# Kernel optimization log

Measured on AMD Instinct MI355X. Metric: run time of the kernel, lower is better.

## Reference

```python
import jax, jax.numpy as jnp
import numpy as np

U, I, K = 100000, 50000, 64
N_II_LAYERS = 2
N_UI_LAYERS = 3
EPS = 1e-12  # torch F.normalize default eps


def spmm(src, dst, w, x, n):
    # out[dst] += w * x[src]  (COO sparse-dense matmul, LGConv with normalize=False)
    return jax.ops.segment_sum(x[src] * w[:, None], dst, num_segments=n)


def l2norm(x):
    # torch.nn.functional.normalize(x, p=2, dim=1)
    return x / jnp.maximum(jnp.linalg.norm(x, axis=1, keepdims=True), EPS)


def setup_inputs() -> dict:
    key = jax.random.key(0)
    ks = jax.random.split(key, 9)
    E_II, E_UI = 1600000, 4800000
    return {
        "Gu": jax.random.normal(ks[0], (U, K), dtype=jnp.float32),
        "Gi": jax.random.normal(ks[1], (I, K), dtype=jnp.float32),
        "Gis": jax.random.normal(ks[2], (I, K), dtype=jnp.float32),
        "ii_w": jax.random.uniform(ks[3], (E_II,), dtype=jnp.float32),
        "ui_w": jax.random.uniform(ks[4], (E_UI,), dtype=jnp.float32),
        "ii_src": jax.random.randint(ks[5], (E_II,), 0, I, dtype=jnp.int32),
        "ii_dst": jax.random.randint(ks[6], (E_II,), 0, I, dtype=jnp.int32),
        "ui_src": jax.random.randint(ks[7], (E_UI,), 0, U + I, dtype=jnp.int32),
        "ui_dst": jax.random.randint(ks[8], (E_UI,), 0, U + I, dtype=jnp.int32),
    }


def reference(Gu, Gi, Gis, ii_w, ui_w, ii_src, ii_dst, ui_src, ui_dst):
    # item-item propagation (n_ii_layers LGConv, no per-layer norm)
    gis = Gis
    for _ in range(N_II_LAYERS):
        gis = spmm(ii_src, ii_dst, ii_w, gis, I)
    # user-item propagation with per-layer L2 normalize
    ego = jnp.concatenate([Gu, Gi], axis=0)  # [U+I, K]
    all_emb = [ego]
    for layer in range(N_UI_LAYERS):
        all_emb.append(l2norm(spmm(ui_src, ui_dst, ui_w, all_emb[layer], U + I)))
    mean_emb = jnp.mean(jnp.stack(all_emb, axis=1), axis=1)  # [U+I, K]
    gu, gi = mean_emb[:U], mean_emb[U:]
    return gu, gi + l2norm(gis)
```

## Files before the change

kernel.cpp:

```cpp
#include <hip/hip_runtime.h>
#include <hip/hip_bf16.h>

constexpr int U_N = 100000;
constexpr int I_N = 50000;
constexpr int KDIM = 64;
constexpr float EPSF = 1e-12f;

constexpr int RPB = 256;
constexpr int BSHIFT = 8;
constexpr int CH = 4096;

typedef float f4 __attribute__((ext_vector_type(4)));
typedef unsigned short u16;

__device__ inline f4 ld4(const float* p) { return *(const f4*)p; }

__device__ inline unsigned pack_bf16(float a, float b) {
    unsigned ua = __float_as_uint(a);
    unsigned ub = __float_as_uint(b);
    ua += 0x7fffu + ((ua >> 16) & 1u);
    ub += 0x7fffu + ((ub >> 16) & 1u);
    return (ua >> 16) | (ub & 0xffff0000u);
}

__device__ inline void bf8_to_f32(uint4 u, float* f) {
    unsigned w0 = u.x, w1 = u.y, w2 = u.z, w3 = u.w;
    f[0] = __uint_as_float(w0 << 16);  f[1] = __uint_as_float(w0 & 0xffff0000u);
    f[2] = __uint_as_float(w1 << 16);  f[3] = __uint_as_float(w1 & 0xffff0000u);
    f[4] = __uint_as_float(w2 << 16);  f[5] = __uint_as_float(w2 & 0xffff0000u);
    f[6] = __uint_as_float(w3 << 16);  f[7] = __uint_as_float(w3 & 0xffff0000u);
}

__global__ void bhist_k(const int* __restrict__ dst, int* __restrict__ cnt, int E, int NB) {
    __shared__ int h[1024];
    int t = threadIdx.x;
    for (int i = t; i < 1024; i += 256) h[i] = 0;
    __syncthreads();
    int stride = gridDim.x * 256 * 4;
    for (int i = (blockIdx.x * 256 + t) * 4; i < E; i += stride) {
        if (i + 4 <= E) {
            int4 d = *(const int4*)(dst + i);
            atomicAdd(&h[d.x >> BSHIFT], 1);
            atomicAdd(&h[d.y >> BSHIFT], 1);
            atomicAdd(&h[d.z >> BSHIFT], 1);
            atomicAdd(&h[d.w >> BSHIFT], 1);
        } else {
            for (int k = i; k < E; ++k) atomicAdd(&h[dst[k] >> BSHIFT], 1);
        }
    }
    __syncthreads();
    for (int i = t; i < NB; i += 256) if (h[i]) atomicAdd(&cnt[i], h[i]);
}

__global__ void bscan_k(const int* __restrict__ cnt, int* __restrict__ base,
                        int* __restrict__ cur, int NB) {
    __shared__ int s[1024];
    int t = threadIdx.x;
    int c = (t < NB) ? cnt[t] : 0;
    s[t] = c;
    __syncthreads();
    for (int off = 1; off < 1024; off <<= 1) {
        int v = s[t] + ((t >= off) ? s[t - off] : 0);
        __syncthreads();
        s[t] = v;
        __syncthreads();
    }
    int ex = s[t] - c;
    if (t < NB) { base[t] = ex; cur[t] = ex; }
    if (t == NB - 1) base[NB] = s[t];
}

__global__ __launch_bounds__(1024) void bpart_k(
        const int* __restrict__ src, const int* __restrict__ dst,
        const float* __restrict__ w, int* __restrict__ gcur,
        int2* __restrict__ pairs, unsigned char* __restrict__ dlo,
        int E, int NB) {
    __shared__ int hist[1024];
    __shared__ int sA[1024];
    __shared__ int rb[1024];
    __shared__ int2 stp[CH];
    __shared__ unsigned stg[CH];
    int t = threadIdx.x;
    int nch = (E + CH - 1) / CH;
    for (int c = blockIdx.x; c < nch; c += gridDim.x) {
        int cb = c * CH;
        int n = min(CH, E - cb);
        hist[t] = 0;
        __syncthreads();
        int esrc[4], ew[4], ebkt[4], edlo[4];
        bool ev[4];
#pragma unroll
        for (int k = 0; k < 4; ++k) {
            int j = k * 1024 + t;
            ev[k] = j < n;
            if (ev[k]) {
                int i = cb + j;
                int d = dst[i];
                esrc[k] = src[i];
                ew[k] = __float_as_int(w[i]);
                ebkt[k] = d >> BSHIFT;
                edlo[k] = d & (RPB - 1);
                atomicAdd(&hist[ebkt[k]], 1);
            }
        }
        __syncthreads();
        int cnt_t = hist[t];
        sA[t] = cnt_t;
        __syncthreads();
        for (int off = 1; off < 1024; off <<= 1) {
            int v = sA[t] + ((t >= off) ? sA[t - off] : 0);
            __syncthreads();
            sA[t] = v;
            __syncthreads();
        }
        sA[t] -= cnt_t;
        if (t < NB && cnt_t > 0) rb[t] = atomicAdd(&gcur[t], cnt_t);
        hist[t] = 0;
        __syncthreads();
#pragma unroll
        for (int k = 0; k < 4; ++k) {
            if (ev[k]) {
                int b = ebkt[k];
                int local = atomicAdd(&hist[b], 1);
                int pos = sA[b] + local;
                stp[pos] = make_int2(esrc[k], ew[k]);
                stg[pos] = (unsigned)(rb[b] + local) | ((unsigned)edlo[k] << 24);
            }
        }
        __syncthreads();
#pragma unroll
        for (int k = 0; k < 4; ++k) {
            int p = k * 1024 + t;
            if (p < n) {
                unsigned g = stg[p];
                unsigned ga = g & 0xFFFFFFu;
                pairs[ga] = stp[p];
                dlo[ga] = (unsigned char)(g >> 24);
            }
        }
        __syncthreads();
    }
}

__global__ __launch_bounds__(1024) void bfill_k(
        const int* __restrict__ base, const int2* __restrict__ pairs,
        const unsigned char* __restrict__ dlo, int2* __restrict__ e2,
        int* __restrict__ start, int NB, int Nrows) {
    __shared__ int hist[RPB];
    __shared__ int pos[RPB + 1];
    int t = threadIdx.x;
    for (int b = blockIdx.x; b < NB; b += gridDim.x) {
        int gb = base[b];
        int cnt = base[b + 1] - gb;
        if (t < RPB) hist[t] = 0;
        __syncthreads();
        for (int i = t; i < cnt; i += 1024) atomicAdd(&hist[dlo[gb + i]], 1);
        __syncthreads();
        if (t < RPB) pos[t] = hist[t];
        __syncthreads();
        for (int off = 1; off < RPB; off <<= 1) {
            int v = 0;
            if (t < RPB) v = pos[t] + ((t >= off) ? pos[t - off] : 0);
            __syncthreads();
            if (t < RPB) pos[t] = v;
            __syncthreads();
        }
        int myv = 0;
        if (t < RPB) myv = (t == 0) ? 0 : pos[t - 1];
        __syncthreads();
        if (t < RPB) pos[t] = myv;
        if (t == 0) pos[RPB] = cnt;
        __syncthreads();
        int r0 = b * RPB;
        if (t <= RPB) {
            int row = r0 + t;
            if (row <= Nrows) start[row] = gb + pos[t];
        }
        __syncthreads();
        for (int i = t; i < cnt; i += 1024) {
            int r = dlo[gb + i];
            int p = atomicAdd(&pos[r], 1);
            e2[gb + p] = pairs[gb + i];
        }
        __syncthreads();
    }
}


__device__ inline float group8_sum(float v) {
    v += __shfl_xor(v, 1, 64);
    v += __shfl_xor(v, 2, 64);
    v += __shfl_xor(v, 4, 64);
    return v;
}

__device__ inline void spmm_row_bf(const int2* __restrict__ e2, int j0, int j1,
                                   const u16* __restrict__ x, int g, int l,
                                   float a[8]) {
    float a0[8] = {0, 0, 0, 0, 0, 0, 0, 0};
    float a1[8] = {0, 0, 0, 0, 0, 0, 0, 0};
    int j = j0;
    for (; j + 16 <= j1; j += 16) {
        int2 ea = e2[j + g];
        int2 eb = e2[j + 8 + g];
        uint4 ua = *(const uint4*)(x + (size_t)ea.x * KDIM + l * 8);
        uint4 ub = *(const uint4*)(x + (size_t)eb.x * KDIM + l * 8);
        float wa = __int_as_float(ea.y), wb = __int_as_float(eb.y);
        float fa[8], fb[8];
        bf8_to_f32(ua, fa);
        bf8_to_f32(ub, fb);
#pragma unroll
        for (int c = 0; c < 8; ++c) {
            a0[c] += wa * fa[c];
            a1[c] += wb * fb[c];
        }
    }
    for (; j < j1; j += 8) {
        if (j + g < j1) {
            int2 ea = e2[j + g];
            uint4 ua = *(const uint4*)(x + (size_t)ea.x * KDIM + l * 8);
            float wa = __int_as_float(ea.y);
            float fa[8];
            bf8_to_f32(ua, fa);
#pragma unroll
            for (int c = 0; c < 8; ++c) a0[c] += wa * fa[c];
        }
    }
#pragma unroll
    for (int c = 0; c < 8; ++c) {
        float v = a0[c] + a1[c];
        v += __shfl_xor(v, 8, 64);
        v += __shfl_xor(v, 16, 64);
        v += __shfl_xor(v, 32, 64);
        a[c] = v;
    }
}

__global__ void cvt_bf8(const float* __restrict__ in, u16* __restrict__ out, int n8) {
    int i = blockIdx.x * blockDim.x + threadIdx.x;
    if (i >= n8) return;
    f4 v0 = ld4(in + (size_t)i * 8);
    f4 v1 = ld4(in + (size_t)i * 8 + 4);
    uint4 pk;
    pk.x = pack_bf16(v0.x, v0.y);
    pk.y = pack_bf16(v0.z, v0.w);
    pk.z = pack_bf16(v1.x, v1.y);
    pk.w = pack_bf16(v1.z, v1.w);
    *(uint4*)(out + (size_t)i * 8) = pk;
}

__global__ void spmm_pull_bf(const int* __restrict__ start, const int2* __restrict__ e2,
                             const u16* __restrict__ x, u16* __restrict__ y, int nrows) {
    const int lane = threadIdx.x & 63;
    const int g = lane >> 3, l = lane & 7;
    const int r = (blockIdx.x * blockDim.x + threadIdx.x) >> 6;
    if (r >= nrows) return;
    float a[8];
    spmm_row_bf(e2, start[r], start[r + 1], x, g, l, a);
    if (g == 0) {
        uint4 pk;
        pk.x = pack_bf16(a[0], a[1]);
        pk.y = pack_bf16(a[2], a[3]);
        pk.z = pack_bf16(a[4], a[5]);
        pk.w = pack_bf16(a[6], a[7]);
        *(uint4*)(y + (size_t)r * KDIM + l * 8) = pk;
    }
}

__global__ void spmm_pull_f32(const int* __restrict__ start, const int2* __restrict__ e2,
                              const u16* __restrict__ x, float* __restrict__ y, int nrows) {
    const int lane = threadIdx.x & 63;
    const int g = lane >> 3, l = lane & 7;
    const int r = (blockIdx.x * blockDim.x + threadIdx.x) >> 6;
    if (r >= nrows) return;
    float a[8];
    spmm_row_bf(e2, start[r], start[r + 1], x, g, l, a);
    if (g == 0) {
        float* yp = y + (size_t)r * KDIM + l * 8;
        *(f4*)yp = f4{a[0], a[1], a[2], a[3]};
        *(f4*)(yp + 4) = f4{a[4], a[5], a[6], a[7]};
    }
}

__global__ void spmm_pull_norm_noacc(const int* __restrict__ start, const int2* __restrict__ e2,
                                     const u16* __restrict__ x, u16* __restrict__ cur,
                                     int nrows) {
    const int lane = threadIdx.x & 63;
    const int g = lane >> 3, l = lane & 7;
    const int r = (blockIdx.x * blockDim.x + threadIdx.x) >> 6;
    if (r >= nrows) return;
    float a[8];
    spmm_row_bf(e2, start[r], start[r + 1], x, g, l, a);
    float loc = 0.f;
#pragma unroll
    for (int c = 0; c < 8; ++c) loc += a[c] * a[c];
    float ss = group8_sum(loc);
    float inv = 1.f / fmaxf(sqrtf(ss), EPSF);
    if (g == 0) {
        uint4 pk;
        pk.x = pack_bf16(a[0] * inv, a[1] * inv);
        pk.y = pack_bf16(a[2] * inv, a[3] * inv);
        pk.z = pack_bf16(a[4] * inv, a[5] * inv);
        pk.w = pack_bf16(a[6] * inv, a[7] * inv);
        *(uint4*)(cur + (size_t)r * KDIM + l * 8) = pk;
    }
}

__global__ void spmm_pull_norm_final(const int* __restrict__ start, const int2* __restrict__ e2,
                                     const u16* __restrict__ x,
                                     const u16* __restrict__ n1,
                                     const float* __restrict__ Gu,
                                     const float* __restrict__ Gi,
                                     const float* __restrict__ gis,
                                     float* __restrict__ out, int nrows) {
    const int lane = threadIdx.x & 63;
    const int g = lane >> 3, l = lane & 7;
    const int r = (blockIdx.x * blockDim.x + threadIdx.x) >> 6;
    if (r >= nrows) return;
    float a[8];
    spmm_row_bf(e2, start[r], start[r + 1], x, g, l, a);
    float loc = 0.f;
#pragma unroll
    for (int c = 0; c < 8; ++c) loc += a[c] * a[c];
    float ss = group8_sum(loc);
    float inv = 1.f / fmaxf(sqrtf(ss), EPSF);
    if (g != 0) return;
    const float* ep = (r < U_N) ? Gu + (size_t)r * KDIM + l * 8
                                : Gi + (size_t)(r - U_N) * KDIM + l * 8;
    f4 e0 = __builtin_nontemporal_load((const f4*)ep);
    f4 e1 = __builtin_nontemporal_load((const f4*)(ep + 4));
    uint4 u1 = *(const uint4*)(n1 + (size_t)r * KDIM + l * 8);
    uint4 u2 = *(const uint4*)(x + (size_t)r * KDIM + l * 8);
    float f1[8], f2[8];
    bf8_to_f32(u1, f1);
    bf8_to_f32(u2, f2);
    f4 v0 = (e0 + f4{f1[0], f1[1], f1[2], f1[3]} + f4{f2[0], f2[1], f2[2], f2[3]}
                + f4{a[0] * inv, a[1] * inv, a[2] * inv, a[3] * inv}) * 0.25f;
    f4 v1 = (e1 + f4{f1[4], f1[5], f1[6], f1[7]} + f4{f2[4], f2[5], f2[6], f2[7]}
                + f4{a[4] * inv, a[5] * inv, a[6] * inv, a[7] * inv}) * 0.25f;
    if (r >= U_N) {
        const float* gp = gis + (size_t)(r - U_N) * KDIM + l * 8;
        f4 g0 = ld4(gp);
        f4 g1 = ld4(gp + 4);
        float loc2 = g0.x * g0.x + g0.y * g0.y + g0.z * g0.z + g0.w * g0.w
                   + g1.x * g1.x + g1.y * g1.y + g1.z * g1.z + g1.w * g1.w;
        float ss2 = group8_sum(loc2);
        float inv2 = 1.f / fmaxf(sqrtf(ss2), EPSF);
        v0 += g0 * inv2;
        v1 += g1 * inv2;
    }
    float* op = out + (size_t)r * KDIM + l * 8;
    __builtin_nontemporal_store(v0, (f4*)op);
    __builtin_nontemporal_store(v1, (f4*)(op + 4));
}

extern "C" void kernel_launch(void* const* d_in, const int* in_sizes, int n_in,
                              void* d_out, int out_size, void* d_ws, size_t ws_size,
                              hipStream_t stream) {
    const float* Gu     = (const float*)d_in[0];
    const float* Gi     = (const float*)d_in[1];
    const float* Gis    = (const float*)d_in[2];
    const float* ii_w   = (const float*)d_in[3];
    const float* ui_w   = (const float*)d_in[4];
    const int*   ii_src = (const int*)d_in[5];
    const int*   ii_dst = (const int*)d_in[6];
    const int*   ui_src = (const int*)d_in[7];
    const int*   ui_dst = (const int*)d_in[8];
    const int E_II = in_sizes[5];
    const int E_UI = in_sizes[7];

    const int NR    = U_N + I_N;
    const size_t NI = (size_t)I_N * KDIM;
    const size_t NA = (size_t)NR * KDIM;

    u16*  bufA = (u16*)d_ws;
    u16*  bufB = bufA + NA;
    u16*  gis0 = bufB + NA;
    u16*  gisA = gis0 + NI;
    float* gisB = (float*)(gisA + NI);
    int2*  ui_e = (int2*)(gisB + NI);
    int2*  ii_e = ui_e + E_UI;
    int*   ui_start = (int*)(ii_e + E_II);
    int*   ii_start = ui_start + (NR + 1);
    int*   bkt_cnt  = ii_start + (I_N + 1);
    int*   bkt_base = bkt_cnt + 1024;
    int*   bkt_cur  = bkt_base + 1056;

    int2*          pairs_s = (int2*)bufA;
    unsigned char* dlo_s   = (unsigned char*)gis0;

    float* out = (float*)d_out;

    const int NB_UI = (NR + RPB - 1) / RPB;
    const int NB_II = (I_N + RPB - 1) / RPB;

    hipMemsetAsync(bkt_cnt, 0, NB_UI * sizeof(int), stream);
    bhist_k<<<1024, 256, 0, stream>>>(ui_dst, bkt_cnt, E_UI, NB_UI);
    bscan_k<<<1, 1024, 0, stream>>>(bkt_cnt, bkt_base, bkt_cur, NB_UI);
    bpart_k<<<512, 1024, 0, stream>>>(ui_src, ui_dst, ui_w, bkt_cur, pairs_s, dlo_s, E_UI, NB_UI);
    bfill_k<<<256, 1024, 0, stream>>>(bkt_base, pairs_s, dlo_s, ui_e, ui_start, NB_UI, NR);

    hipMemsetAsync(bkt_cnt, 0, NB_II * sizeof(int), stream);
    bhist_k<<<1024, 256, 0, stream>>>(ii_dst, bkt_cnt, E_II, NB_II);
    bscan_k<<<1, 1024, 0, stream>>>(bkt_cnt, bkt_base, bkt_cur, NB_II);
    bpart_k<<<512, 1024, 0, stream>>>(ii_src, ii_dst, ii_w, bkt_cur, pairs_s, dlo_s, E_II, NB_II);
    bfill_k<<<256, 1024, 0, stream>>>(bkt_base, pairs_s, dlo_s, ii_e, ii_start, NB_II, I_N);

    cvt_bf8<<<(int)((NI / 8 + 255) / 256), 256, 0, stream>>>(Gis, gis0, (int)(NI / 8));
    spmm_pull_bf<<<(I_N + 3) / 4, 256, 0, stream>>>(ii_start, ii_e, gis0, gisA, I_N);
    spmm_pull_f32<<<(I_N + 3) / 4, 256, 0, stream>>>(ii_start, ii_e, gisA, gisB, I_N);

    const int nu8 = (int)((size_t)U_N * KDIM / 8);
    const int ni8 = (int)(NI / 8);
    cvt_bf8<<<(nu8 + 255) / 256, 256, 0, stream>>>(Gu, bufA, nu8);
    cvt_bf8<<<(ni8 + 255) / 256, 256, 0, stream>>>(Gi, bufA + (size_t)U_N * KDIM, ni8);

    spmm_pull_norm_noacc<<<(NR + 3) / 4, 256, 0, stream>>>(ui_start, ui_e, bufA, bufB, NR);
    spmm_pull_norm_noacc<<<(NR + 3) / 4, 256, 0, stream>>>(ui_start, ui_e, bufB, bufA, NR);
    spmm_pull_norm_final<<<(NR + 3) / 4, 256, 0, stream>>>(ui_start, ui_e, bufA, bufB,
                                                           Gu, Gi, gisB, out, NR);
}
```

Measured before the change: 686.6 us.

## Fuse item-item and user-item SpMM layers into shared launches; unroll gather deeper

```diff
diff --git a/kernel.cpp b/kernel.cpp
--- a/kernel.cpp
+++ b/kernel.cpp
@@ -11,9 +11,21 @@
 constexpr int CH = 4096;
 
 typedef float f4 __attribute__((ext_vector_type(4)));
+typedef int   i2v __attribute__((ext_vector_type(2)));
+typedef unsigned uv4 __attribute__((ext_vector_type(4)));
 typedef unsigned short u16;
 
 __device__ inline f4 ld4(const float* p) { return *(const f4*)p; }
+
+__device__ inline i2v ntl_e(const int2* p) {
+    return __builtin_nontemporal_load((const i2v*)p);
+}
+__device__ inline uv4 ntl_u4(const u16* p) {
+    return __builtin_nontemporal_load((const uv4*)p);
+}
+__device__ inline f4 ntl_f4(const float* p) {
+    return __builtin_nontemporal_load((const f4*)p);
+}
 
 __device__ inline unsigned pack_bf16(float a, float b) {
     unsigned ua = __float_as_uint(a);
@@ -23,12 +35,18 @@
     return (ua >> 16) | (ub & 0xffff0000u);
 }
 
-__device__ inline void bf8_to_f32(uint4 u, float* f) {
-    unsigned w0 = u.x, w1 = u.y, w2 = u.z, w3 = u.w;
-    f[0] = __uint_as_float(w0 << 16);  f[1] = __uint_as_float(w0 & 0xffff0000u);
-    f[2] = __uint_as_float(w1 << 16);  f[3] = __uint_as_float(w1 & 0xffff0000u);
-    f[4] = __uint_as_float(w2 << 16);  f[5] = __uint_as_float(w2 & 0xffff0000u);
-    f[6] = __uint_as_float(w3 << 16);  f[7] = __uint_as_float(w3 & 0xffff0000u);
+__device__ inline void bf8_to_f32(uv4 u, float* f) {
+    f[0] = __uint_as_float(u[0] << 16);  f[1] = __uint_as_float(u[0] & 0xffff0000u);
+    f[2] = __uint_as_float(u[1] << 16);  f[3] = __uint_as_float(u[1] & 0xffff0000u);
+    f[4] = __uint_as_float(u[2] << 16);  f[5] = __uint_as_float(u[2] & 0xffff0000u);
+    f[6] = __uint_as_float(u[3] << 16);  f[7] = __uint_as_float(u[3] & 0xffff0000u);
+}
+
+__device__ inline void fma8(float A[8], float w, uv4 u) {
+    float f[8];
+    bf8_to_f32(u, f);
+#pragma unroll
+    for (int c = 0; c < 8; ++c) A[c] += w * f[c];
 }
 
 __global__ void bhist_k(const int* __restrict__ dst, int* __restrict__ cnt, int E, int NB) {
@@ -194,41 +212,47 @@
     return v;
 }
 
-__device__ inline void spmm_row_bf(const int2* __restrict__ e2, int j0, int j1,
+__device__ inline void spmm_row_bf(const int2* __restrict__ e2p, int j0, int j1,
                                    const u16* __restrict__ x, int g, int l,
                                    float a[8]) {
-    float a0[8] = {0, 0, 0, 0, 0, 0, 0, 0};
-    float a1[8] = {0, 0, 0, 0, 0, 0, 0, 0};
+    float A0[8] = {0, 0, 0, 0, 0, 0, 0, 0};
+    float A1[8] = {0, 0, 0, 0, 0, 0, 0, 0};
+    float A2[8] = {0, 0, 0, 0, 0, 0, 0, 0};
+    float A3[8] = {0, 0, 0, 0, 0, 0, 0, 0};
     int j = j0;
-    for (; j + 16 <= j1; j += 16) {
-        int2 ea = e2[j + g];
-        int2 eb = e2[j + 8 + g];
-        uint4 ua = *(const uint4*)(x + (size_t)ea.x * KDIM + l * 8);
-        uint4 ub = *(const uint4*)(x + (size_t)eb.x * KDIM + l * 8);
-        float wa = __int_as_float(ea.y), wb = __int_as_float(eb.y);
-        float fa[8], fb[8];
-        bf8_to_f32(ua, fa);
-        bf8_to_f32(ub, fb);
-#pragma unroll
-        for (int c = 0; c < 8; ++c) {
-            a0[c] += wa * fa[c];
-            a1[c] += wb * fb[c];
-        }
+    for (; j + 32 <= j1; j += 32) {
+        i2v e0 = ntl_e(e2p + j + g);
+        i2v e1 = ntl_e(e2p + j + 8 + g);
+        i2v e2 = ntl_e(e2p + j + 16 + g);
+        i2v e3 = ntl_e(e2p + j + 24 + g);
+        uv4 u0 = *(const uv4*)(x + (size_t)e0.x * KDIM + l * 8);
+        uv4 u1 = *(const uv4*)(x + (size_t)e1.x * KDIM + l * 8);
+        uv4 u2 = *(const uv4*)(x + (size_t)e2.x * KDIM + l * 8);
+        uv4 u3 = *(const uv4*)(x + (size_t)e3.x * KDIM + l * 8);
+        fma8(A0, __int_as_float(e0.y), u0);
+        fma8(A1, __int_as_float(e1.y), u1);
+        fma8(A2, __int_as_float(e2.y), u2);
+        fma8(A3, __int_as_float(e3.y), u3);
+    }
+    if (j + 16 <= j1) {
+        i2v e0 = ntl_e(e2p + j + g);
+        i2v e1 = ntl_e(e2p + j + 8 + g);
+        uv4 u0 = *(const uv4*)(x + (size_t)e0.x * KDIM + l * 8);
+        uv4 u1 = *(const uv4*)(x + (size_t)e1.x * KDIM + l * 8);
+        fma8(A0, __int_as_float(e0.y), u0);
+        fma8(A1, __int_as_float(e1.y), u1);
+        j += 16;
     }
     for (; j < j1; j += 8) {
         if (j + g < j1) {
-            int2 ea = e2[j + g];
-            uint4 ua = *(const uint4*)(x + (size_t)ea.x * KDIM + l * 8);
-            float wa = __int_as_float(ea.y);
-            float fa[8];
-            bf8_to_f32(ua, fa);
-#pragma unroll
-            for (int c = 0; c < 8; ++c) a0[c] += wa * fa[c];
+            i2v e0 = ntl_e(e2p + j + g);
+            uv4 u0 = *(const uv4*)(x + (size_t)e0.x * KDIM + l * 8);
+            fma8(A2, __int_as_float(e0.y), u0);
         }
     }
 #pragma unroll
     for (int c = 0; c < 8; ++c) {
-        float v = a0[c] + a1[c];
+        float v = (A0[c] + A1[c]) + (A2[c] + A3[c]);
         v += __shfl_xor(v, 8, 64);
         v += __shfl_xor(v, 16, 64);
         v += __shfl_xor(v, 32, 64);
@@ -236,73 +260,98 @@
     }
 }
 
-__global__ void cvt_bf8(const float* __restrict__ in, u16* __restrict__ out, int n8) {
+__global__ void cvt_all(const float* __restrict__ Gu, const float* __restrict__ Gi,
+                        const float* __restrict__ Gis, u16* __restrict__ bufA,
+                        u16* __restrict__ gis0, int nu8, int na8, int ntot8) {
     int i = blockIdx.x * blockDim.x + threadIdx.x;
-    if (i >= n8) return;
-    f4 v0 = ld4(in + (size_t)i * 8);
-    f4 v1 = ld4(in + (size_t)i * 8 + 4);
-    uint4 pk;
-    pk.x = pack_bf16(v0.x, v0.y);
-    pk.y = pack_bf16(v0.z, v0.w);
-    pk.z = pack_bf16(v1.x, v1.y);
-    pk.w = pack_bf16(v1.z, v1.w);
-    *(uint4*)(out + (size_t)i * 8) = pk;
-}
-
-__global__ void spmm_pull_bf(const int* __restrict__ start, const int2* __restrict__ e2,
-                             const u16* __restrict__ x, u16* __restrict__ y, int nrows) {
+    if (i >= ntot8) return;
+    const float* p;
+    u16* o;
+    if (i < nu8)      { p = Gu  + (size_t)i * 8;          o = bufA + (size_t)i * 8; }
+    else if (i < na8) { p = Gi  + (size_t)(i - nu8) * 8;  o = bufA + (size_t)i * 8; }
+    else              { p = Gis + (size_t)(i - na8) * 8;  o = gis0 + (size_t)(i - na8) * 8; }
+    f4 v0 = ld4(p);
+    f4 v1 = ld4(p + 4);
+    uv4 pk;
+    pk[0] = pack_bf16(v0.x, v0.y);
+    pk[1] = pack_bf16(v0.z, v0.w);
+    pk[2] = pack_bf16(v1.x, v1.y);
+    pk[3] = pack_bf16(v1.z, v1.w);
+    *(uv4*)o = pk;
+}
+
+__global__ void spmm_fused_l1(const int* __restrict__ ui_start, const int2* __restrict__ ui_e,
+                              const u16* __restrict__ xu, u16* __restrict__ yu,
+                              const int* __restrict__ ii_start, const int2* __restrict__ ii_e,
+                              const u16* __restrict__ xi, u16* __restrict__ yi,
+                              int nui, int nii) {
     const int lane = threadIdx.x & 63;
     const int g = lane >> 3, l = lane & 7;
     const int r = (blockIdx.x * blockDim.x + threadIdx.x) >> 6;
-    if (r >= nrows) return;
-    float a[8];
-    spmm_row_bf(e2, start[r], start[r + 1], x, g, l, a);
-    if (g == 0) {
-        uint4 pk;
-        pk.x = pack_bf16(a[0], a[1]);
-        pk.y = pack_bf16(a[2], a[3]);
-        pk.z = pack_bf16(a[4], a[5]);
-        pk.w = pack_bf16(a[6], a[7]);
-        *(uint4*)(y + (size_t)r * KDIM + l * 8) = pk;
-    }
-}
-
-__global__ void spmm_pull_f32(const int* __restrict__ start, const int2* __restrict__ e2,
-                              const u16* __restrict__ x, float* __restrict__ y, int nrows) {
+    if (r < nui) {
+        float a[8];
+        spmm_row_bf(ui_e, ui_start[r], ui_start[r + 1], xu, g, l, a);
+        float loc = 0.f;
+#pragma unroll
+        for (int c = 0; c < 8; ++c) loc += a[c] * a[c];
+        float ss = group8_sum(loc);
+        float inv = 1.f / fmaxf(sqrtf(ss), EPSF);
+        if (g == 0) {
+            uv4 pk;
+            pk[0] = pack_bf16(a[0] * inv, a[1] * inv);
+            pk[1] = pack_bf16(a[2] * inv, a[3] * inv);
+            pk[2] = pack_bf16(a[4] * inv, a[5] * inv);
+            pk[3] = pack_bf16(a[6] * inv, a[7] * inv);
+            *(uv4*)(yu + (size_t)r * KDIM + l * 8) = pk;
+        }
+    } else if (r < nui + nii) {
+        int rr = r - nui;
+        float a[8];
+        spmm_row_bf(ii_e, ii_start[rr], ii_start[rr + 1], xi, g, l, a);
+        if (g == 0) {
+            uv4 pk;
+            pk[0] = pack_bf16(a[0], a[1]);
+            pk[1] = pack_bf16(a[2], a[3]);
+            pk[2] = pack_bf16(a[4], a[5]);
+            pk[3] = pack_bf16(a[6], a[7]);
+            *(uv4*)(yi + (size_t)rr * KDIM + l * 8) = pk;
+        }
+    }
+}
+
+__global__ void spmm_fused_l2(const int* __restrict__ ui_start, const int2* __restrict__ ui_e,
+                              const u16* __restrict__ xu, u16* __restrict__ yu,
+                              const int* __restrict__ ii_start, const int2* __restrict__ ii_e,
+                              const u16* __restrict__ xi, float* __restrict__ yi,
+                              int nui, int nii) {
     const int lane = threadIdx.x & 63;
     const int g = lane >> 3, l = lane & 7;
     const int r = (blockIdx.x * blockDim.x + threadIdx.x) >> 6;
-    if (r >= nrows) return;
-    float a[8];
-    spmm_row_bf(e2, start[r], start[r + 1], x, g, l, a);
-    if (g == 0) {
-        float* yp = y + (size_t)r * KDIM + l * 8;
-        *(f4*)yp = f4{a[0], a[1], a[2], a[3]};
-        *(f4*)(yp + 4) = f4{a[4], a[5], a[6], a[7]};
-    }
-}
-
-__global__ void spmm_pull_norm_noacc(const int* __restrict__ start, const int2* __restrict__ e2,
-                                     const u16* __restrict__ x, u16* __restrict__ cur,
-                                     int nrows) {
-    const int lane = threadIdx.x & 63;
-    const int g = lane >> 3, l = lane & 7;
-    const int r = (blockIdx.x * blockDim.x + threadIdx.x) >> 6;
-    if (r >= nrows) return;
-    float a[8];
-    spmm_row_bf(e2, start[r], start[r + 1], x, g, l, a);
-    float loc = 0.f;
-#pragma unroll
-    for (int c = 0; c < 8; ++c) loc += a[c] * a[c];
-    float ss = group8_sum(loc);
-    float inv = 1.f / fmaxf(sqrtf(ss), EPSF);
-    if (g == 0) {
-        uint4 pk;
-        pk.x = pack_bf16(a[0] * inv, a[1] * inv);
-        pk.y = pack_bf16(a[2] * inv, a[3] * inv);
-        pk.z = pack_bf16(a[4] * inv, a[5] * inv);
-        pk.w = pack_bf16(a[6] * inv, a[7] * inv);
-        *(uint4*)(cur + (size_t)r * KDIM + l * 8) = pk;
+    if (r < nui) {
+        float a[8];
+        spmm_row_bf(ui_e, ui_start[r], ui_start[r + 1], xu, g, l, a);
+        float loc = 0.f;
+#pragma unroll
+        for (int c = 0; c < 8; ++c) loc += a[c] * a[c];
+        float ss = group8_sum(loc);
+        float inv = 1.f / fmaxf(sqrtf(ss), EPSF);
+        if (g == 0) {
+            uv4 pk;
+            pk[0] = pack_bf16(a[0] * inv, a[1] * inv);
+            pk[1] = pack_bf16(a[2] * inv, a[3] * inv);
+            pk[2] = pack_bf16(a[4] * inv, a[5] * inv);
+            pk[3] = pack_bf16(a[6] * inv, a[7] * inv);
+            *(uv4*)(yu + (size_t)r * KDIM + l * 8) = pk;
+        }
+    } else if (r < nui + nii) {
+        int rr = r - nui;
+        float a[8];
+        spmm_row_bf(ii_e, ii_start[rr], ii_start[rr + 1], xi, g, l, a);
+        if (g == 0) {
+            float* yp = yi + (size_t)rr * KDIM + l * 8;
+            *(f4*)yp = f4{a[0], a[1], a[2], a[3]};
+            *(f4*)(yp + 4) = f4{a[4], a[5], a[6], a[7]};
+        }
     }
 }
 
@@ -327,10 +376,10 @@
     if (g != 0) return;
     const float* ep = (r < U_N) ? Gu + (size_t)r * KDIM + l * 8
                                 : Gi + (size_t)(r - U_N) * KDIM + l * 8;
-    f4 e0 = __builtin_nontemporal_load((const f4*)ep);
-    f4 e1 = __builtin_nontemporal_load((const f4*)(ep + 4));
-    uint4 u1 = *(const uint4*)(n1 + (size_t)r * KDIM + l * 8);
-    uint4 u2 = *(const uint4*)(x + (size_t)r * KDIM + l * 8);
+    f4 e0 = ntl_f4(ep);
+    f4 e1 = ntl_f4(ep + 4);
+    uv4 u1 = ntl_u4(n1 + (size_t)r * KDIM + l * 8);
+    uv4 u2 = *(const uv4*)(x + (size_t)r * KDIM + l * 8);
     float f1[8], f2[8];
     bf8_to_f32(u1, f1);
     bf8_to_f32(u2, f2);
@@ -340,8 +389,8 @@
                 + f4{a[4] * inv, a[5] * inv, a[6] * inv, a[7] * inv}) * 0.25f;
     if (r >= U_N) {
         const float* gp = gis + (size_t)(r - U_N) * KDIM + l * 8;
-        f4 g0 = ld4(gp);
-        f4 g1 = ld4(gp + 4);
+        f4 g0 = ntl_f4(gp);
+        f4 g1 = ntl_f4(gp + 4);
         float loc2 = g0.x * g0.x + g0.y * g0.y + g0.z * g0.z + g0.w * g0.w
                    + g1.x * g1.x + g1.y * g1.y + g1.z * g1.z + g1.w * g1.w;
         float ss2 = group8_sum(loc2);
@@ -406,17 +455,16 @@
     bpart_k<<<512, 1024, 0, stream>>>(ii_src, ii_dst, ii_w, bkt_cur, pairs_s, dlo_s, E_II, NB_II);
     bfill_k<<<256, 1024, 0, stream>>>(bkt_base, pairs_s, dlo_s, ii_e, ii_start, NB_II, I_N);
 
-    cvt_bf8<<<(int)((NI / 8 + 255) / 256), 256, 0, stream>>>(Gis, gis0, (int)(NI / 8));
-    spmm_pull_bf<<<(I_N + 3) / 4, 256, 0, stream>>>(ii_start, ii_e, gis0, gisA, I_N);
-    spmm_pull_f32<<<(I_N + 3) / 4, 256, 0, stream>>>(ii_start, ii_e, gisA, gisB, I_N);
-
     const int nu8 = (int)((size_t)U_N * KDIM / 8);
-    const int ni8 = (int)(NI / 8);
-    cvt_bf8<<<(nu8 + 255) / 256, 256, 0, stream>>>(Gu, bufA, nu8);
-    cvt_bf8<<<(ni8 + 255) / 256, 256, 0, stream>>>(Gi, bufA + (size_t)U_N * KDIM, ni8);
-
-    spmm_pull_norm_noacc<<<(NR + 3) / 4, 256, 0, stream>>>(ui_start, ui_e, bufA, bufB, NR);
-    spmm_pull_norm_noacc<<<(NR + 3) / 4, 256, 0, stream>>>(ui_start, ui_e, bufB, bufA, NR);
+    const int na8 = (int)(NA / 8);
+    const int nt8 = (int)((NA + NI) / 8);
+    cvt_all<<<(nt8 + 255) / 256, 256, 0, stream>>>(Gu, Gi, Gis, bufA, gis0, nu8, na8, nt8);
+
+    const int NTOT = NR + I_N;
+    spmm_fused_l1<<<(NTOT + 3) / 4, 256, 0, stream>>>(ui_start, ui_e, bufA, bufB,
+                                                      ii_start, ii_e, gis0, gisA, NR, I_N);
+    spmm_fused_l2<<<(NTOT + 3) / 4, 256, 0, stream>>>(ui_start, ui_e, bufB, bufA,
+                                                      ii_start, ii_e, gisA, gisB, NR, I_N);
     spmm_pull_norm_final<<<(NR + 3) / 4, 256, 0, stream>>>(ui_start, ui_e, bufA, bufB,
                                                            Gu, Gi, gisB, out, NR);
 }
```

Measured after the change: 829.1 us. 20.8% more time.

## Batch UI and II CSR construction into shared launches and pack row index into weight bits

Applied to the files above, without the earlier changes.

```diff
diff --git a/kernel.cpp b/kernel.cpp
--- a/kernel.cpp
+++ b/kernel.cpp
@@ -31,13 +31,18 @@
     f[6] = __uint_as_float(w3 << 16);  f[7] = __uint_as_float(w3 & 0xffff0000u);
 }
 
-__global__ void bhist_k(const int* __restrict__ dst, int* __restrict__ cnt, int E, int NB) {
+__global__ void bhist2_k(const int* __restrict__ dstU, int* __restrict__ cntU, int EU, int NBu,
+                         const int* __restrict__ dstI, int* __restrict__ cntI, int EI, int NBi,
+                         int GU, int GTOT) {
+    const int* dst; int* cnt; int E; int NB; int nbk; int bid;
+    if ((int)blockIdx.x < GU) { dst = dstU; cnt = cntU; E = EU; NB = NBu; nbk = GU; bid = blockIdx.x; }
+    else { dst = dstI; cnt = cntI; E = EI; NB = NBi; nbk = GTOT - GU; bid = blockIdx.x - GU; }
     __shared__ int h[1024];
     int t = threadIdx.x;
     for (int i = t; i < 1024; i += 256) h[i] = 0;
     __syncthreads();
-    int stride = gridDim.x * 256 * 4;
-    for (int i = (blockIdx.x * 256 + t) * 4; i < E; i += stride) {
+    int stride = nbk * 256 * 4;
+    for (int i = (bid * 256 + t) * 4; i < E; i += stride) {
         if (i + 4 <= E) {
             int4 d = *(const int4*)(dst + i);
             atomicAdd(&h[d.x >> BSHIFT], 1);
@@ -52,11 +57,13 @@
     for (int i = t; i < NB; i += 256) if (h[i]) atomicAdd(&cnt[i], h[i]);
 }
 
-__global__ void bscan_k(const int* __restrict__ cnt, int* __restrict__ base,
-                        int* __restrict__ cur, int NB) {
+__global__ void bscan2_k(const int* __restrict__ cntU, int* __restrict__ baseU,
+                         int* __restrict__ curU, int NBu,
+                         const int* __restrict__ cntI, int* __restrict__ baseI,
+                         int* __restrict__ curI, int NBi) {
     __shared__ int s[1024];
     int t = threadIdx.x;
-    int c = (t < NB) ? cnt[t] : 0;
+    int c = (t < NBu) ? cntU[t] : 0;
     s[t] = c;
     __syncthreads();
     for (int off = 1; off < 1024; off <<= 1) {
@@ -65,29 +72,47 @@
         s[t] = v;
         __syncthreads();
     }
-    int ex = s[t] - c;
-    if (t < NB) { base[t] = ex; cur[t] = ex; }
-    if (t == NB - 1) base[NB] = s[t];
-}
-
-__global__ __launch_bounds__(1024) void bpart_k(
-        const int* __restrict__ src, const int* __restrict__ dst,
-        const float* __restrict__ w, int* __restrict__ gcur,
-        int2* __restrict__ pairs, unsigned char* __restrict__ dlo,
-        int E, int NB) {
+    if (t < NBu) { baseU[t] = s[t] - c; curU[t] = s[t] - c; }
+    if (t == NBu - 1) baseU[NBu] = s[t];
+    __syncthreads();
+    int c2 = (t < NBi) ? cntI[t] : 0;
+    s[t] = c2;
+    __syncthreads();
+    for (int off = 1; off < 1024; off <<= 1) {
+        int v = s[t] + ((t >= off) ? s[t - off] : 0);
+        __syncthreads();
+        s[t] = v;
+        __syncthreads();
+    }
+    if (t < NBi) { baseI[t] = s[t] - c2; curI[t] = s[t] - c2; }
+    if (t == NBi - 1) baseI[NBi] = s[t];
+}
+
+__global__ __launch_bounds__(1024) void bpart2_k(
+        const int* __restrict__ srcU, const int* __restrict__ dstU,
+        const float* __restrict__ wU, int* __restrict__ curU,
+        int2* __restrict__ pairsU, int nchU, int EU,
+        const int* __restrict__ srcI, const int* __restrict__ dstI,
+        const float* __restrict__ wI, int* __restrict__ curI,
+        int2* __restrict__ pairsI, int nchI, int EI) {
     __shared__ int hist[1024];
     __shared__ int sA[1024];
     __shared__ int rb[1024];
     __shared__ int2 stp[CH];
     __shared__ unsigned stg[CH];
     int t = threadIdx.x;
-    int nch = (E + CH - 1) / CH;
-    for (int c = blockIdx.x; c < nch; c += gridDim.x) {
-        int cb = c * CH;
+    int ntot = nchU + nchI;
+    for (int c = blockIdx.x; c < ntot; c += gridDim.x) {
+        const int* src; const int* dst; const float* w; int* gcur; int2* pairs;
+        int cb, E;
+        if (c < nchU) { src = srcU; dst = dstU; w = wU; gcur = curU; pairs = pairsU;
+                        cb = c * CH; E = EU; }
+        else          { src = srcI; dst = dstI; w = wI; gcur = curI; pairs = pairsI;
+                        cb = (c - nchU) * CH; E = EI; }
         int n = min(CH, E - cb);
         hist[t] = 0;
         __syncthreads();
-        int esrc[4], ew[4], ebkt[4], edlo[4];
+        int esrc[4], ew[4], ebkt[4];
         bool ev[4];
 #pragma unroll
         for (int k = 0; k < 4; ++k) {
@@ -97,9 +122,8 @@
                 int i = cb + j;
                 int d = dst[i];
                 esrc[k] = src[i];
-                ew[k] = __float_as_int(w[i]);
+                ew[k] = (int)((__float_as_uint(w[i]) & 0xFFFFFF00u) | (unsigned)(d & (RPB - 1)));
                 ebkt[k] = d >> BSHIFT;
-                edlo[k] = d & (RPB - 1);
                 atomicAdd(&hist[ebkt[k]], 1);
             }
         }
@@ -114,7 +138,7 @@
             __syncthreads();
         }
         sA[t] -= cnt_t;
-        if (t < NB && cnt_t > 0) rb[t] = atomicAdd(&gcur[t], cnt_t);
+        if (cnt_t > 0) rb[t] = atomicAdd(&gcur[t], cnt_t);
         hist[t] = 0;
         __syncthreads();
 #pragma unroll
@@ -124,37 +148,39 @@
                 int local = atomicAdd(&hist[b], 1);
                 int pos = sA[b] + local;
                 stp[pos] = make_int2(esrc[k], ew[k]);
-                stg[pos] = (unsigned)(rb[b] + local) | ((unsigned)edlo[k] << 24);
+                stg[pos] = (unsigned)(rb[b] + local);
             }
         }
         __syncthreads();
 #pragma unroll
         for (int k = 0; k < 4; ++k) {
             int p = k * 1024 + t;
-            if (p < n) {
-                unsigned g = stg[p];
-                unsigned ga = g & 0xFFFFFFu;
-                pairs[ga] = stp[p];
-                dlo[ga] = (unsigned char)(g >> 24);
-            }
-        }
-        __syncthreads();
-    }
-}
-
-__global__ __launch_bounds__(1024) void bfill_k(
-        const int* __restrict__ base, const int2* __restrict__ pairs,
-        const unsigned char* __restrict__ dlo, int2* __restrict__ e2,
-        int* __restrict__ start, int NB, int Nrows) {
+            if (p < n) pairs[stg[p]] = stp[p];
+        }
+        __syncthreads();
+    }
+}
+
+__global__ __launch_bounds__(1024) void bfill2_k(
+        const int* __restrict__ baseU, const int2* __restrict__ pairsU,
+        int2* __restrict__ e2U, int* __restrict__ startU, int NBu, int NRu,
+        const int* __restrict__ baseI, const int2* __restrict__ pairsI,
+        int2* __restrict__ e2I, int* __restrict__ startI, int NBi, int NRi) {
     __shared__ int hist[RPB];
     __shared__ int pos[RPB + 1];
     int t = threadIdx.x;
-    for (int b = blockIdx.x; b < NB; b += gridDim.x) {
-        int gb = base[b];
-        int cnt = base[b + 1] - gb;
+    int ntot = NBu + NBi;
+    for (int b = blockIdx.x; b < ntot; b += gridDim.x) {
+        const int* base; const int2* pairs; int2* e2; int* start; int bb, Nrows;
+        if (b < NBu) { base = baseU; pairs = pairsU; e2 = e2U; start = startU;
+                       bb = b; Nrows = NRu; }
+        else         { base = baseI; pairs = pairsI; e2 = e2I; start = startI;
+                       bb = b - NBu; Nrows = NRi; }
+        int gb = base[bb];
+        int cnt = base[bb + 1] - gb;
         if (t < RPB) hist[t] = 0;
         __syncthreads();
-        for (int i = t; i < cnt; i += 1024) atomicAdd(&hist[dlo[gb + i]], 1);
+        for (int i = t; i < cnt; i += 1024) atomicAdd(&hist[pairs[gb + i].y & (RPB - 1)], 1);
         __syncthreads();
         if (t < RPB) pos[t] = hist[t];
         __syncthreads();
@@ -171,16 +197,17 @@
         if (t < RPB) pos[t] = myv;
         if (t == 0) pos[RPB] = cnt;
         __syncthreads();
-        int r0 = b * RPB;
+        int r0 = bb * RPB;
         if (t <= RPB) {
             int row = r0 + t;
             if (row <= Nrows) start[row] = gb + pos[t];
         }
         __syncthreads();
         for (int i = t; i < cnt; i += 1024) {
-            int r = dlo[gb + i];
+            int2 pe = pairs[gb + i];
+            int r = pe.y & (RPB - 1);
             int p = atomicAdd(&pos[r], 1);
-            e2[gb + p] = pairs[gb + i];
+            e2[gb + p] = make_int2(pe.x, pe.y & ~(RPB - 1));
         }
         __syncthreads();
     }
@@ -236,17 +263,24 @@
     }
 }
 
-__global__ void cvt_bf8(const float* __restrict__ in, u16* __restrict__ out, int n8) {
+__global__ void cvt_all(const float* __restrict__ Gu, const float* __restrict__ Gi,
+                        const float* __restrict__ Gis, u16* __restrict__ bufA,
+                        u16* __restrict__ gis0, int nu8, int na8, int ntot8) {
     int i = blockIdx.x * blockDim.x + threadIdx.x;
-    if (i >= n8) return;
-    f4 v0 = ld4(in + (size_t)i * 8);
-    f4 v1 = ld4(in + (size_t)i * 8 + 4);
+    if (i >= ntot8) return;
+    const float* p;
+    u16* o;
+    if (i < nu8)      { p = Gu  + (size_t)i * 8;          o = bufA + (size_t)i * 8; }
+    else if (i < na8) { p = Gi  + (size_t)(i - nu8) * 8;  o = bufA + (size_t)i * 8; }
+    else              { p = Gis + (size_t)(i - na8) * 8;  o = gis0 + (size_t)(i - na8) * 8; }
+    f4 v0 = ld4(p);
+    f4 v1 = ld4(p + 4);
     uint4 pk;
     pk.x = pack_bf16(v0.x, v0.y);
     pk.y = pack_bf16(v0.z, v0.w);
     pk.z = pack_bf16(v1.x, v1.y);
     pk.w = pack_bf16(v1.z, v1.w);
-    *(uint4*)(out + (size_t)i * 8) = pk;
+    *(uint4*)o = pk;
 }
 
 __global__ void spmm_pull_bf(const int* __restrict__ start, const int2* __restrict__ e2,
@@ -386,34 +420,40 @@
     int*   bkt_base = bkt_cnt + 1024;
     int*   bkt_cur  = bkt_base + 1056;
 
-    int2*          pairs_s = (int2*)bufA;
-    unsigned char* dlo_s   = (unsigned char*)gis0;
+    int2* pairsU = (int2*)bufA;
+    int2* pairsI = (int2*)gis0;
 
     float* out = (float*)d_out;
 
     const int NB_UI = (NR + RPB - 1) / RPB;
     const int NB_II = (I_N + RPB - 1) / RPB;
-
-    hipMemsetAsync(bkt_cnt, 0, NB_UI * sizeof(int), stream);
-    bhist_k<<<1024, 256, 0, stream>>>(ui_dst, bkt_cnt, E_UI, NB_UI);
-    bscan_k<<<1, 1024, 0, stream>>>(bkt_cnt, bkt_base, bkt_cur, NB_UI);
-    bpart_k<<<512, 1024, 0, stream>>>(ui_src, ui_dst, ui_w, bkt_cur, pairs_s, dlo_s, E_UI, NB_UI);
-    bfill_k<<<256, 1024, 0, stream>>>(bkt_base, pairs_s, dlo_s, ui_e, ui_start, NB_UI, NR);
-
-    hipMemsetAsync(bkt_cnt, 0, NB_II * sizeof(int), stream);
-    bhist_k<<<1024, 256, 0, stream>>>(ii_dst, bkt_cnt, E_II, NB_II);
-    bscan_k<<<1, 1024, 0, stream>>>(bkt_cnt, bkt_base, bkt_cur, NB_II);
-    bpart_k<<<512, 1024, 0, stream>>>(ii_src, ii_dst, ii_w, bkt_cur, pairs_s, dlo_s, E_II, NB_II);
-    bfill_k<<<256, 1024, 0, stream>>>(bkt_base, pairs_s, dlo_s, ii_e, ii_start, NB_II, I_N);
-
-    cvt_bf8<<<(int)((NI / 8 + 255) / 256), 256, 0, stream>>>(Gis, gis0, (int)(NI / 8));
+    int* cntU  = bkt_cnt;
+    int* cntI  = bkt_cnt + NB_UI;
+    int* baseU = bkt_base;
+    int* baseI = bkt_base + (NB_UI + 1);
+    int* curU  = bkt_cur;
+    int* curI  = bkt_cur + NB_UI;
+
+    const int nchU = (E_UI + CH - 1) / CH;
+    const int nchI = (E_II + CH - 1) / CH;
+
+    hipMemsetAsync(bkt_cnt, 0, (NB_UI + NB_II) * sizeof(int), stream);
+    bhist2_k<<<1024, 256, 0, stream>>>(ui_dst, cntU, E_UI, NB_UI,
+                                       ii_dst, cntI, E_II, NB_II, 768, 1024);
+    bscan2_k<<<1, 1024, 0, stream>>>(cntU, baseU, curU, NB_UI,
+                                     cntI, baseI, curI, NB_II);
+    bpart2_k<<<512, 1024, 0, stream>>>(ui_src, ui_dst, ui_w, curU, pairsU, nchU, E_UI,
+                                       ii_src, ii_dst, ii_w, curI, pairsI, nchI, E_II);
+    bfill2_k<<<512, 1024, 0, stream>>>(baseU, pairsU, ui_e, ui_start, NB_UI, NR,
+                                       baseI, pairsI, ii_e, ii_start, NB_II, I_N);
+
+    const int nu8 = (int)((size_t)U_N * KDIM / 8);
+    const int na8 = (int)(NA / 8);
+    const int nt8 = (int)((NA + NI) / 8);
+    cvt_all<<<(nt8 + 255) / 256, 256, 0, stream>>>(Gu, Gi, Gis, bufA, gis0, nu8, na8, nt8);
+
     spmm_pull_bf<<<(I_N + 3) / 4, 256, 0, stream>>>(ii_start, ii_e, gis0, gisA, I_N);
     spmm_pull_f32<<<(I_N + 3) / 4, 256, 0, stream>>>(ii_start, ii_e, gisA, gisB, I_N);
-
-    const int nu8 = (int)((size_t)U_N * KDIM / 8);
-    const int ni8 = (int)(NI / 8);
-    cvt_bf8<<<(nu8 + 255) / 256, 256, 0, stream>>>(Gu, bufA, nu8);
-    cvt_bf8<<<(ni8 + 255) / 256, 256, 0, stream>>>(Gi, bufA + (size_t)U_N * KDIM, ni8);
 
     spmm_pull_norm_noacc<<<(NR + 3) / 4, 256, 0, stream>>>(ui_start, ui_e, bufA, bufB, NR);
     spmm_pull_norm_noacc<<<(NR + 3) / 4, 256, 0, stream>>>(ui_start, ui_e, bufB, bufA, NR);
```

Measured after the change: 622.4 us. 1.1x faster.
